# Kernel optimization log

Hardware: AMD Instinct MI355X
Metric: run time of the kernel (lower is better)

The kernel has to match this reference:

```python
import jax, jax.numpy as jnp
import numpy as np

B, S, D, E, H = 8, 1024, 1024, 8, 4096  # batch, seq, n_embd, num_experts, 4*n_embd


def setup_inputs() -> dict:
    key = jax.random.key(0)
    ks = jax.random.split(key, 8)
    sc = 0.02
    return {
        "x": jax.random.normal(ks[0], (B, S, D), jnp.float32),
        "noise": jax.random.normal(ks[1], (B, S, E), jnp.float32),
        "Wg": jax.random.normal(ks[2], (D, E), jnp.float32) * sc,
        "bg": jnp.zeros((E,), jnp.float32),
        "Wn": jax.random.normal(ks[3], (D, E), jnp.float32) * sc,
        "bn": jnp.zeros((E,), jnp.float32),
        "W1": jax.random.normal(ks[4], (E, D, H), jnp.float32) * sc,
        "b1": jnp.zeros((E, H), jnp.float32),
        "W2": jax.random.normal(ks[5], (E, H, D), jnp.float32) * sc,
        "b2": jnp.zeros((E, D), jnp.float32),
        "top_k": 2,
    }


def reference(x, noise, Wg, bg, Wn, bn, W1, b1, W2, b2, top_k):
    # --- NoisyTopkRouter ---
    logits = jnp.einsum("bsd,de->bse", x, Wg) + bg
    noise_logits = jnp.einsum("bsd,de->bse", x, Wn) + bn
    noisy = logits + noise * jax.nn.softplus(noise_logits)  # [B,S,E]
    _, idx = jax.lax.top_k(noisy, top_k)  # [B,S,K]
    in_topk = jax.nn.one_hot(idx, noisy.shape[-1], dtype=noisy.dtype).sum(-2) > 0
    sparse_logits = jnp.where(in_topk, noisy, -jnp.inf)
    gating = jax.nn.softmax(sparse_logits, axis=-1)  # zero outside top-k

    # --- dispatch/combine: gating is exactly zero for non-selected experts,
    # so per-expert masked gather + weighted scatter-add == gated dense sum ---
    g_e = jnp.moveaxis(gating, -1, 0)  # [E,B,S]

    def body(acc, params):
        W1e, b1e, W2e, b2e, ge = params
        h = jax.nn.relu(jnp.einsum("bsd,dh->bsh", x, W1e) + b1e)  # [B,S,H]
        y = (jnp.einsum("bsh,hd->bsd", h, W2e) + b2e) * ge[..., None]
        return acc + y, y

    final_output, expert_outputs = jax.lax.scan(
        body, jnp.zeros_like(x), (W1, b1, W2, b2, g_e)
    )
    # expert_outputs: [E,B,S,D], matching the per-expert weighted outputs list
    return final_output, expert_outputs, gating
```

## Files before the change

### kernel.cpp

```cpp
#include <hip/hip_runtime.h>
#include <hip/hip_bf16.h>
#include <stdint.h>

#define TKN   8192
#define DD    1024
#define EE    8
#define HH    4096
#define TOPK  2
#define NASG  (TKN * TOPK)
#define NSLOT 72

typedef unsigned short u16;
typedef __bf16 bf16x8 __attribute__((ext_vector_type(8)));
typedef float  f32x4  __attribute__((ext_vector_type(4)));

__device__ __forceinline__ u16 f2bf(float f) {
  __hip_bfloat16 h = __float2bfloat16(f);
  return __builtin_bit_cast(u16, h);
}

__device__ __forceinline__ void glds16(const void* g, void* l) {
  __builtin_amdgcn_global_load_lds(
      (__attribute__((address_space(1))) void*)g,
      (__attribute__((address_space(3))) void*)l, 16, 0, 0);
}

#define FENCE() asm volatile("" ::: "memory")
#define BAR()   do { FENCE(); __builtin_amdgcn_s_barrier(); FENCE(); } while (0)
#define VMCNT8() asm volatile("s_waitcnt vmcnt(8)" ::: "memory")
#define VMCNT0() asm volatile("s_waitcnt vmcnt(0)" ::: "memory")

__global__ __launch_bounds__(256) void transpose_cvt_kernel(
    const float* __restrict__ src, u16* __restrict__ dst, int R, int C) {
  __shared__ float tile[32][33];
  int e = blockIdx.z;
  int c0 = blockIdx.x * 32, r0 = blockIdx.y * 32;
  int tx = threadIdx.x, ty = threadIdx.y;
  const float* s = src + (size_t)e * R * C;
  u16* d = dst + (size_t)e * R * C;
#pragma unroll
  for (int j = 0; j < 4; j++)
    tile[ty * 4 + j][tx] = s[(size_t)(r0 + ty * 4 + j) * C + c0 + tx];
  __syncthreads();
#pragma unroll
  for (int j = 0; j < 4; j++)
    d[(size_t)(c0 + ty * 4 + j) * R + r0 + tx] = f2bf(tile[tx][ty * 4 + j]);
}

__global__ __launch_bounds__(256) void router_kernel(
    const float* __restrict__ x, const float* __restrict__ noise,
    const float* __restrict__ Wg, const float* __restrict__ bg,
    const float* __restrict__ Wn, const float* __restrict__ bn,
    float* __restrict__ gating, u16* __restrict__ xb,
    int* __restrict__ sel_e, float* __restrict__ sel_g) {
  int t = blockIdx.x;
  int tid = threadIdx.x;
  float acc[16];
#pragma unroll
  for (int j = 0; j < 16; j++) acc[j] = 0.f;
  for (int i = tid; i < DD; i += 256) {
    float xv = x[(size_t)t * DD + i];
    xb[(size_t)t * DD + i] = f2bf(xv);
    const float4* g4 = (const float4*)(Wg + (size_t)i * EE);
    const float4* n4 = (const float4*)(Wn + (size_t)i * EE);
    float4 ga = g4[0], gb = g4[1];
    float4 na = n4[0], nb = n4[1];
    acc[0] += xv * ga.x;  acc[1] += xv * ga.y;  acc[2] += xv * ga.z;  acc[3] += xv * ga.w;
    acc[4] += xv * gb.x;  acc[5] += xv * gb.y;  acc[6] += xv * gb.z;  acc[7] += xv * gb.w;
    acc[8] += xv * na.x;  acc[9] += xv * na.y;  acc[10] += xv * na.z; acc[11] += xv * na.w;
    acc[12] += xv * nb.x; acc[13] += xv * nb.y; acc[14] += xv * nb.z; acc[15] += xv * nb.w;
  }
  __shared__ float red[4][16];
  int lane = tid & 63, wv = tid >> 6;
#pragma unroll
  for (int j = 0; j < 16; j++) {
    float v = acc[j];
    for (int o = 32; o > 0; o >>= 1) v += __shfl_down(v, o);
    acc[j] = v;
  }
  if (lane == 0) {
#pragma unroll
    for (int j = 0; j < 16; j++) red[wv][j] = acc[j];
  }
  __syncthreads();
  if (tid == 0) {
    float nz[EE];
#pragma unroll
    for (int e = 0; e < EE; e++) {
      float dg = red[0][e] + red[1][e] + red[2][e] + red[3][e] + bg[e];
      float dn = red[0][8 + e] + red[1][8 + e] + red[2][8 + e] + red[3][8 + e] + bn[e];
      float sp = fmaxf(dn, 0.f) + log1pf(expf(-fabsf(dn)));
      nz[e] = dg + noise[(size_t)t * EE + e] * sp;
    }
    int m1 = 0;
    for (int e = 1; e < EE; e++) if (nz[e] > nz[m1]) m1 = e;
    int m2 = (m1 == 0) ? 1 : 0;
    for (int e = 0; e < EE; e++) if (e != m1 && nz[e] > nz[m2]) m2 = e;
    float eb = expf(nz[m2] - nz[m1]);
    float den = 1.f + eb;
    float g1 = 1.f / den, g2 = eb / den;
    gating[(size_t)t * EE + m1] = g1;
    gating[(size_t)t * EE + m2] = g2;
    sel_e[t * 2] = m1; sel_e[t * 2 + 1] = m2;
    sel_g[t * 2] = g1; sel_g[t * 2 + 1] = g2;
  }
}

__global__ __launch_bounds__(256) void hist_scan_kernel(
    const int* __restrict__ sel_e, int* __restrict__ counts,
    int* __restrict__ offsets, int* __restrict__ cursors,
    int* __restrict__ slots) {
  __shared__ int hist[EE];
  int tid = threadIdx.x;
  if (tid < EE) hist[tid] = 0;
  __syncthreads();
  for (int i = tid; i < NASG; i += 256) atomicAdd(&hist[sel_e[i]], 1);
  __syncthreads();
  if (tid == 0) {
    int off = 0, ns = 0;
    for (int e = 0; e < EE; e++) {
      int c = hist[e];
      counts[e] = c; offsets[e] = off; cursors[e] = off; off += c;
      int nrt = (c + 255) >> 8;
      for (int rt = 0; rt < nrt; rt++) slots[ns++] = (e << 16) | rt;
    }
    for (; ns < NSLOT; ns++) slots[ns] = -1;
  }
}

__global__ __launch_bounds__(256) void build_lists_kernel(
    const int* __restrict__ sel_e, const float* __restrict__ sel_g,
    int* __restrict__ cursors, int* __restrict__ tok_list,
    float* __restrict__ gate_list) {
  int t = blockIdx.x * 256 + threadIdx.x;
  int lane = threadIdx.x & 63;
#pragma unroll
  for (int k = 0; k < TOPK; k++) {
    int e = sel_e[t * 2 + k];
    float g = sel_g[t * 2 + k];
    for (int ee = 0; ee < EE; ee++) {
      unsigned long long m = __ballot(e == ee);
      if (m) {
        int leader = __ffsll(m) - 1;
        int base = 0;
        if (lane == leader) base = atomicAdd(&cursors[ee], __popcll(m));
        base = __shfl(base, leader);
        if (e == ee) {
          int slot = base + __popcll(m & ((1ull << lane) - 1ull));
          tok_list[slot] = t;
          gate_list[slot] = g;
        }
      }
    }
  }
}

__global__ __launch_bounds__(256) void zerofill_kernel(
    const float* __restrict__ gating, float* __restrict__ expert_out) {
  int id = blockIdx.x;
  int e = id >> 13, t = id & (TKN - 1);
  if (gating[(size_t)t * EE + e] != 0.f) return;
  float4* p = (float4*)(expert_out + ((size_t)e * TKN + t) * DD);
  p[threadIdx.x] = (float4){0.f, 0.f, 0.f, 0.f};
}

__global__ __launch_bounds__(256) void combine_kernel(
    const float* __restrict__ expert_out, const int* __restrict__ sel_e,
    float* __restrict__ final_out) {
  int t = blockIdx.x;
  int e1 = sel_e[2 * t], e2 = sel_e[2 * t + 1];
  const float4* r1 = (const float4*)(expert_out + ((size_t)e1 * TKN + t) * DD);
  const float4* r2 = (const float4*)(expert_out + ((size_t)e2 * TKN + t) * DD);
  float4* o = (float4*)(final_out + (size_t)t * DD);
  int i = threadIdx.x;
  float4 a = r1[i], b = r2[i];
  o[i] = (float4){a.x + b.x, a.y + b.y, a.z + b.z, a.w + b.w};
}

template<int KLEN, bool GATHER, bool EPI2, int LOGC>
__global__ __launch_bounds__(512, 2) void gemm8_kernel(
    const u16* __restrict__ A, const u16* __restrict__ Bm,
    const float* __restrict__ bias, const int* __restrict__ tok_list,
    const float* __restrict__ gate_list, const int* __restrict__ counts,
    const int* __restrict__ offsets, const int* __restrict__ slots,
    int Ncols, u16* __restrict__ OutBf, float* __restrict__ expert_out) {
  constexpr int NT = KLEN / 64;
  int gid = blockIdx.x;
  int q = gid >> 3;
  int slot = (gid & 7) * 9 + (q >> LOGC);
  int ct = q & ((1 << LOGC) - 1);
  int packed = slots[slot];
  if (packed < 0) return;
  int e = packed >> 16;
  int rt = packed & 0xffff;
  int cnt = counts[e];
  int off = offsets[e];
  int col0 = ct * 256;

  __shared__ __attribute__((aligned(16))) char ldsc[131072];

  int tid = threadIdx.x;
  int w = tid >> 6, l = tid & 63;
  int wm = w >> 2, wn = w & 3;
  int fr = l & 15, hi = l >> 4;
  int kk16 = hi << 4;
  int xr = (fr & 7) << 4;

  int rl0 = w * 8 + (l >> 3);
  int slotE = ((l & 7) ^ ((l >> 3) & 7)) << 3;
  const u16* aptr[4];
  const u16* bptr[4];
#pragma unroll
  for (int i = 0; i < 4; i++) {
    int r = rt * 256 + rl0 + i * 64;
    if (GATHER) {
      int idx = min(off + r, NASG - 1);
      aptr[i] = A + (size_t)tok_list[idx] * KLEN + slotE;
    } else {
      aptr[i] = A + (size_t)(off + r) * KLEN + slotE;
    }
    bptr[i] = Bm + ((size_t)e * Ncols + col0 + rl0 + i * 64) * KLEN + slotE;
  }
  char* ldsA = ldsc;
  char* ldsB = ldsc + 65536;

  auto issueA = [&](int t, int h) {
    char* d = ldsA + (t & 1) * 32768 + h * 16384 + w * 1024;
    glds16(aptr[h * 2 + 0] + t * 64, d);
    glds16(aptr[h * 2 + 1] + t * 64, d + 8192);
  };
  auto issueB = [&](int t, int h) {
    char* d = ldsB + (t & 1) * 32768 + h * 16384 + w * 1024;
    glds16(bptr[h * 2 + 0] + t * 64, d);
    glds16(bptr[h * 2 + 1] + t * 64, d + 8192);
  };

  f32x4 acc[8][4];
#pragma unroll
  for (int m = 0; m < 8; m++)
#pragma unroll
    for (int n = 0; n < 4; n++) acc[m][n] = (f32x4){0.f, 0.f, 0.f, 0.f};
  bf16x8 aF[4][2], bF0[2][2], bF1[2][2];

  issueB(0, 0); issueB(0, 1); issueA(0, 0); issueA(0, 1);
  issueB(1, 0); issueB(1, 1); issueA(1, 0); issueA(1, 1);
  VMCNT8();
  BAR();

  for (int t = 0; t < NT; t++) {
    int abase = (t & 1) * 32768;
    int bbase = 65536 + (t & 1) * 32768;
#pragma unroll
    for (int mm = 0; mm < 4; mm++)
#pragma unroll
      for (int ks = 0; ks < 2; ks++)
        aF[mm][ks] = *(const bf16x8*)(ldsc + abase + (wm * 128 + mm * 16 + fr) * 128 +
                                      ((ks * 64 + kk16) ^ xr));
#pragma unroll
    for (int nn = 0; nn < 2; nn++)
#pragma unroll
      for (int ks = 0; ks < 2; ks++)
        bF0[nn][ks] = *(const bf16x8*)(ldsc + bbase + (wn * 64 + nn * 16 + fr) * 128 +
                                       ((ks * 64 + kk16) ^ xr));
    BAR();
    __builtin_amdgcn_s_setprio(1);
#pragma unroll
    for (int mm = 0; mm < 4; mm++)
#pragma unroll
      for (int nn = 0; nn < 2; nn++)
#pragma unroll
        for (int ks = 0; ks < 2; ks++)
          acc[mm][nn] = __builtin_amdgcn_mfma_f32_16x16x32_bf16(aF[mm][ks], bF0[nn][ks], acc[mm][nn], 0, 0, 0);
    __builtin_amdgcn_s_setprio(0);
    BAR();
#pragma unroll
    for (int nn = 0; nn < 2; nn++)
#pragma unroll
      for (int ks = 0; ks < 2; ks++)
        bF1[nn][ks] = *(const bf16x8*)(ldsc + bbase + (wn * 64 + 32 + nn * 16 + fr) * 128 +
                                       ((ks * 64 + kk16) ^ xr));
    BAR();
    __builtin_amdgcn_s_setprio(1);
#pragma unroll
    for (int mm = 0; mm < 4; mm++)
#pragma unroll
      for (int nn = 0; nn < 2; nn++)
#pragma unroll
        for (int ks = 0; ks < 2; ks++)
          acc[mm][2 + nn] = __builtin_amdgcn_mfma_f32_16x16x32_bf16(aF[mm][ks], bF1[nn][ks], acc[mm][2 + nn], 0, 0, 0);
    __builtin_amdgcn_s_setprio(0);
    BAR();
#pragma unroll
    for (int mm = 0; mm < 4; mm++)
#pragma unroll
      for (int ks = 0; ks < 2; ks++)
        aF[mm][ks] = *(const bf16x8*)(ldsc + abase + (wm * 128 + 64 + mm * 16 + fr) * 128 +
                                      ((ks * 64 + kk16) ^ xr));
    if (t + 2 < NT) { issueB(t + 2, 0); issueB(t + 2, 1); }
    BAR();
    __builtin_amdgcn_s_setprio(1);
#pragma unroll
    for (int mm = 0; mm < 4; mm++)
#pragma unroll
      for (int nn = 0; nn < 2; nn++)
#pragma unroll
        for (int ks = 0; ks < 2; ks++)
          acc[4 + mm][nn] = __builtin_amdgcn_mfma_f32_16x16x32_bf16(aF[mm][ks], bF0[nn][ks], acc[4 + mm][nn], 0, 0, 0);
    __builtin_amdgcn_s_setprio(0);
    BAR();
    if (t + 2 < NT) {
      issueA(t + 2, 0); issueA(t + 2, 1);
      VMCNT8();
    } else {
      VMCNT0();
    }
    BAR();
    __builtin_amdgcn_s_setprio(1);
#pragma unroll
    for (int mm = 0; mm < 4; mm++)
#pragma unroll
      for (int nn = 0; nn < 2; nn++)
#pragma unroll
        for (int ks = 0; ks < 2; ks++)
          acc[4 + mm][2 + nn] = __builtin_amdgcn_mfma_f32_16x16x32_bf16(aF[mm][ks], bF1[nn][ks], acc[4 + mm][2 + nn], 0, 0, 0);
    __builtin_amdgcn_s_setprio(0);
    BAR();
  }

  float biasN[4];
  int cN[4];
#pragma unroll
  for (int n = 0; n < 4; n++) {
    cN[n] = col0 + wn * 64 + (n >> 1) * 32 + (n & 1) * 16 + fr;
    biasN[n] = bias[e * Ncols + cN[n]];
  }
  if constexpr (!EPI2) {
#pragma unroll
    for (int m = 0; m < 8; m++) {
      int rb = rt * 256 + wm * 128 + (m >> 2) * 64 + (m & 3) * 16 + hi * 4;
#pragma unroll
      for (int j = 0; j < 4; j++) {
        int r = rb + j;
        if (r < cnt) {
#pragma unroll
          for (int n = 0; n < 4; n++) {
            float v = acc[m][n][j] + biasN[n];
            OutBf[(size_t)(off + r) * Ncols + cN[n]] = f2bf(fmaxf(v, 0.f));
          }
        }
      }
    }
  } else {
#pragma unroll
    for (int m = 0; m < 8; m++) {
      int rb = rt * 256 + wm * 128 + (m >> 2) * 64 + (m & 3) * 16 + hi * 4;
#pragma unroll
      for (int j = 0; j < 4; j++) {
        int r = rb + j;
        if (r < cnt) {
          int idx = off + r;
          int tok = tok_list[idx];
          float g = gate_list[idx];
          size_t erow = ((size_t)e * TKN + tok) * DD;
#pragma unroll
          for (int n = 0; n < 4; n++)
            expert_out[erow + cN[n]] = (acc[m][n][j] + biasN[n]) * g;
        }
      }
    }
  }
}

extern "C" void kernel_launch(void* const* d_in, const int* in_sizes, int n_in,
                              void* d_out, int out_size, void* d_ws, size_t ws_size,
                              hipStream_t stream) {
  const float* x     = (const float*)d_in[0];
  const float* noise = (const float*)d_in[1];
  const float* Wg    = (const float*)d_in[2];
  const float* bg    = (const float*)d_in[3];
  const float* Wn    = (const float*)d_in[4];
  const float* bn    = (const float*)d_in[5];
  const float* W1    = (const float*)d_in[6];
  const float* b1    = (const float*)d_in[7];
  const float* W2    = (const float*)d_in[8];
  const float* b2    = (const float*)d_in[9];

  float* final_out  = (float*)d_out;
  float* expert_out = final_out + (size_t)TKN * DD;
  float* gating     = expert_out + (size_t)EE * TKN * DD;

  char* ws = (char*)d_ws;
  size_t o = 0;
  auto alloc = [&](size_t bytes) {
    char* p = ws + o;
    o += bytes;
    o = (o + 255) & ~(size_t)255;
    return p;
  };
  u16*   xb        = (u16*)alloc((size_t)TKN * DD * 2);
  u16*   w1t       = (u16*)alloc((size_t)EE * HH * DD * 2);
  u16*   w2t       = (u16*)alloc((size_t)EE * DD * HH * 2);
  u16*   hbuf      = (u16*)alloc(((size_t)NASG + 256) * HH * 2);
  int*   tok_list  = (int*)alloc((size_t)NASG * 4);
  float* gate_list = (float*)alloc((size_t)NASG * 4);
  int*   sel_e     = (int*)alloc((size_t)NASG * 4);
  float* sel_g     = (float*)alloc((size_t)NASG * 4);
  int*   counts    = (int*)alloc(256);
  int*   offsets   = (int*)alloc(256);
  int*   cursors   = (int*)alloc(256);
  int*   slots     = (int*)alloc(NSLOT * 4);

  hipMemsetAsync(gating, 0, (size_t)TKN * EE * sizeof(float), stream);

  router_kernel<<<TKN, 256, 0, stream>>>(x, noise, Wg, bg, Wn, bn, gating, xb, sel_e, sel_g);
  hist_scan_kernel<<<1, 256, 0, stream>>>(sel_e, counts, offsets, cursors, slots);
  build_lists_kernel<<<TKN / 256, 256, 0, stream>>>(sel_e, sel_g, cursors, tok_list, gate_list);
  zerofill_kernel<<<EE * TKN, 256, 0, stream>>>(gating, expert_out);

  transpose_cvt_kernel<<<dim3(HH / 32, DD / 32, EE), dim3(32, 8), 0, stream>>>(W1, w1t, DD, HH);
  transpose_cvt_kernel<<<dim3(DD / 32, HH / 32, EE), dim3(32, 8), 0, stream>>>(W2, w2t, HH, DD);

  gemm8_kernel<DD, true, false, 4><<<8 * 9 * 16, 512, 0, stream>>>(
      xb, w1t, b1, tok_list, nullptr, counts, offsets, slots, HH, hbuf, nullptr);
  gemm8_kernel<HH, false, true, 2><<<8 * 9 * 4, 512, 0, stream>>>(
      hbuf, w2t, b2, tok_list, gate_list, counts, offsets, slots, DD, nullptr, expert_out);

  combine_kernel<<<TKN, 256, 0, stream>>>(expert_out, sel_e, final_out);
}
```

Baseline: 670.5 us.

## Split-K the second expert GEMM and merge partials in a fused combine kernel

The down-projection GEMM is split into four K chunks, which quadruples its block count to fill more CUs. Each chunk writes fp32 partial sums to a workspace buffer. A new merge kernel sums the partials, adds the bias, applies the gate, and writes both the expert outputs and the final combined output. The weight transpose-convert kernel is also widened to 64-row tiles with packed 32-bit bf16 stores. The cost is about 256MB of extra partial-sum traffic, and the old path is kept as a fallback when the workspace is too small.

After: 668.1 us. About the same (-0.3%).

```diff
diff --git a/kernel.cpp b/kernel.cpp
--- a/kernel.cpp
+++ b/kernel.cpp
@@ -32,19 +32,23 @@
 
 __global__ __launch_bounds__(256) void transpose_cvt_kernel(
     const float* __restrict__ src, u16* __restrict__ dst, int R, int C) {
-  __shared__ float tile[32][33];
+  __shared__ float tile[64][33];
   int e = blockIdx.z;
-  int c0 = blockIdx.x * 32, r0 = blockIdx.y * 32;
+  int c0 = blockIdx.x * 32, r0 = blockIdx.y * 64;
   int tx = threadIdx.x, ty = threadIdx.y;
   const float* s = src + (size_t)e * R * C;
-  u16* d = dst + (size_t)e * R * C;
-#pragma unroll
-  for (int j = 0; j < 4; j++)
-    tile[ty * 4 + j][tx] = s[(size_t)(r0 + ty * 4 + j) * C + c0 + tx];
+  uint32_t* d32 = (uint32_t*)(dst + (size_t)e * R * C);
+#pragma unroll
+  for (int j = 0; j < 8; j++)
+    tile[ty * 8 + j][tx] = s[(size_t)(r0 + ty * 8 + j) * C + c0 + tx];
   __syncthreads();
 #pragma unroll
-  for (int j = 0; j < 4; j++)
-    d[(size_t)(c0 + ty * 4 + j) * R + r0 + tx] = f2bf(tile[tx][ty * 4 + j]);
+  for (int jj = 0; jj < 4; jj++) {
+    int c = c0 + ty * 4 + jj;
+    uint32_t lo = f2bf(tile[2 * tx][ty * 4 + jj]);
+    uint32_t hi = f2bf(tile[2 * tx + 1][ty * 4 + jj]);
+    d32[((size_t)c * R + r0) / 2 + tx] = lo | (hi << 16);
+  }
 }
 
 __global__ __launch_bounds__(256) void router_kernel(
@@ -131,7 +135,7 @@
 __global__ __launch_bounds__(256) void build_lists_kernel(
     const int* __restrict__ sel_e, const float* __restrict__ sel_g,
     int* __restrict__ cursors, int* __restrict__ tok_list,
-    float* __restrict__ gate_list) {
+    float* __restrict__ gate_list, int* __restrict__ asg_of) {
   int t = blockIdx.x * 256 + threadIdx.x;
   int lane = threadIdx.x & 63;
 #pragma unroll
@@ -149,6 +153,7 @@
           int slot = base + __popcll(m & ((1ull << lane) - 1ull));
           tok_list[slot] = t;
           gate_list[slot] = g;
+          asg_of[t * 2 + k] = slot;
         }
       }
     }
@@ -177,18 +182,49 @@
   o[i] = (float4){a.x + b.x, a.y + b.y, a.z + b.z, a.w + b.w};
 }
 
-template<int KLEN, bool GATHER, bool EPI2, int LOGC>
+__global__ __launch_bounds__(256) void merge_combine_kernel(
+    const float* __restrict__ part, const int* __restrict__ asg_of,
+    const int* __restrict__ sel_e, const float* __restrict__ sel_g,
+    const float* __restrict__ b2, float* __restrict__ expert_out,
+    float* __restrict__ final_out) {
+  int t = blockIdx.x;
+  int i = threadIdx.x;
+  int i1 = asg_of[2 * t], i2 = asg_of[2 * t + 1];
+  int e1 = sel_e[2 * t], e2 = sel_e[2 * t + 1];
+  float g1 = sel_g[2 * t], g2 = sel_g[2 * t + 1];
+  float4 s1 = {0.f, 0.f, 0.f, 0.f}, s2 = {0.f, 0.f, 0.f, 0.f};
+#pragma unroll
+  for (int kq = 0; kq < 4; kq++) {
+    float4 a = ((const float4*)(part + ((size_t)kq * NASG + i1) * DD))[i];
+    float4 b = ((const float4*)(part + ((size_t)kq * NASG + i2) * DD))[i];
+    s1.x += a.x; s1.y += a.y; s1.z += a.z; s1.w += a.w;
+    s2.x += b.x; s2.y += b.y; s2.z += b.z; s2.w += b.w;
+  }
+  float4 bb1 = ((const float4*)(b2 + (size_t)e1 * DD))[i];
+  float4 bb2 = ((const float4*)(b2 + (size_t)e2 * DD))[i];
+  float4 y1 = {(s1.x + bb1.x) * g1, (s1.y + bb1.y) * g1, (s1.z + bb1.z) * g1, (s1.w + bb1.w) * g1};
+  float4 y2 = {(s2.x + bb2.x) * g2, (s2.y + bb2.y) * g2, (s2.z + bb2.z) * g2, (s2.w + bb2.w) * g2};
+  ((float4*)(expert_out + ((size_t)e1 * TKN + t) * DD))[i] = y1;
+  ((float4*)(expert_out + ((size_t)e2 * TKN + t) * DD))[i] = y2;
+  ((float4*)(final_out + (size_t)t * DD))[i] =
+      (float4){y1.x + y2.x, y1.y + y2.y, y1.z + y2.z, y1.w + y2.w};
+}
+
+template<int KLOOP, int KSTRIDE, bool GATHER, int EPI, int LOGC, int LOGK>
 __global__ __launch_bounds__(512, 2) void gemm8_kernel(
     const u16* __restrict__ A, const u16* __restrict__ Bm,
     const float* __restrict__ bias, const int* __restrict__ tok_list,
     const float* __restrict__ gate_list, const int* __restrict__ counts,
     const int* __restrict__ offsets, const int* __restrict__ slots,
-    int Ncols, u16* __restrict__ OutBf, float* __restrict__ expert_out) {
-  constexpr int NT = KLEN / 64;
+    int Ncols, u16* __restrict__ OutBf, float* __restrict__ outF) {
+  constexpr int NT = KLOOP / 64;
   int gid = blockIdx.x;
   int q = gid >> 3;
-  int slot = (gid & 7) * 9 + (q >> LOGC);
-  int ct = q & ((1 << LOGC) - 1);
+  constexpr int PERX = 9 << LOGC;
+  int kq = q / PERX;
+  int r0q = q - kq * PERX;
+  int slot = (gid & 7) * 9 + (r0q >> LOGC);
+  int ct = r0q & ((1 << LOGC) - 1);
   int packed = slots[slot];
   if (packed < 0) return;
   int e = packed >> 16;
@@ -196,6 +232,7 @@
   int cnt = counts[e];
   int off = offsets[e];
   int col0 = ct * 256;
+  int k0e = kq * KLOOP;
 
   __shared__ __attribute__((aligned(16))) char ldsc[131072];
 
@@ -215,11 +252,11 @@
     int r = rt * 256 + rl0 + i * 64;
     if (GATHER) {
       int idx = min(off + r, NASG - 1);
-      aptr[i] = A + (size_t)tok_list[idx] * KLEN + slotE;
+      aptr[i] = A + (size_t)tok_list[idx] * KSTRIDE + k0e + slotE;
     } else {
-      aptr[i] = A + (size_t)(off + r) * KLEN + slotE;
-    }
-    bptr[i] = Bm + ((size_t)e * Ncols + col0 + rl0 + i * 64) * KLEN + slotE;
+      aptr[i] = A + (size_t)(off + r) * KSTRIDE + k0e + slotE;
+    }
+    bptr[i] = Bm + ((size_t)e * Ncols + col0 + rl0 + i * 64) * KSTRIDE + k0e + slotE;
   }
   char* ldsA = ldsc;
   char* ldsB = ldsc + 65536;
@@ -332,9 +369,9 @@
 #pragma unroll
   for (int n = 0; n < 4; n++) {
     cN[n] = col0 + wn * 64 + (n >> 1) * 32 + (n & 1) * 16 + fr;
-    biasN[n] = bias[e * Ncols + cN[n]];
-  }
-  if constexpr (!EPI2) {
+    biasN[n] = (EPI == 2) ? 0.f : bias[e * Ncols + cN[n]];
+  }
+  if constexpr (EPI == 0) {
 #pragma unroll
     for (int m = 0; m < 8; m++) {
       int rb = rt * 256 + wm * 128 + (m >> 2) * 64 + (m & 3) * 16 + hi * 4;
@@ -350,7 +387,7 @@
         }
       }
     }
-  } else {
+  } else if constexpr (EPI == 1) {
 #pragma unroll
     for (int m = 0; m < 8; m++) {
       int rb = rt * 256 + wm * 128 + (m >> 2) * 64 + (m & 3) * 16 + hi * 4;
@@ -364,7 +401,22 @@
           size_t erow = ((size_t)e * TKN + tok) * DD;
 #pragma unroll
           for (int n = 0; n < 4; n++)
-            expert_out[erow + cN[n]] = (acc[m][n][j] + biasN[n]) * g;
+            outF[erow + cN[n]] = (acc[m][n][j] + biasN[n]) * g;
+        }
+      }
+    }
+  } else {
+#pragma unroll
+    for (int m = 0; m < 8; m++) {
+      int rb = rt * 256 + wm * 128 + (m >> 2) * 64 + (m & 3) * 16 + hi * 4;
+#pragma unroll
+      for (int j = 0; j < 4; j++) {
+        int r = rb + j;
+        if (r < cnt) {
+          size_t prow = ((size_t)kq * NASG + off + r) * DD;
+#pragma unroll
+          for (int n = 0; n < 4; n++)
+            outF[prow + cN[n]] = acc[m][n][j];
         }
       }
     }
@@ -405,25 +457,36 @@
   float* gate_list = (float*)alloc((size_t)NASG * 4);
   int*   sel_e     = (int*)alloc((size_t)NASG * 4);
   float* sel_g     = (float*)alloc((size_t)NASG * 4);
+  int*   asg_of    = (int*)alloc((size_t)NASG * 4);
   int*   counts    = (int*)alloc(256);
   int*   offsets   = (int*)alloc(256);
   int*   cursors   = (int*)alloc(256);
   int*   slots     = (int*)alloc(NSLOT * 4);
+  float* part      = (float*)alloc((size_t)4 * NASG * DD * 4);
+  bool use_split = (o <= ws_size);
 
   hipMemsetAsync(gating, 0, (size_t)TKN * EE * sizeof(float), stream);
 
   router_kernel<<<TKN, 256, 0, stream>>>(x, noise, Wg, bg, Wn, bn, gating, xb, sel_e, sel_g);
   hist_scan_kernel<<<1, 256, 0, stream>>>(sel_e, counts, offsets, cursors, slots);
-  build_lists_kernel<<<TKN / 256, 256, 0, stream>>>(sel_e, sel_g, cursors, tok_list, gate_list);
+  build_lists_kernel<<<TKN / 256, 256, 0, stream>>>(sel_e, sel_g, cursors, tok_list,
+                                                    gate_list, asg_of);
   zerofill_kernel<<<EE * TKN, 256, 0, stream>>>(gating, expert_out);
 
-  transpose_cvt_kernel<<<dim3(HH / 32, DD / 32, EE), dim3(32, 8), 0, stream>>>(W1, w1t, DD, HH);
-  transpose_cvt_kernel<<<dim3(DD / 32, HH / 32, EE), dim3(32, 8), 0, stream>>>(W2, w2t, HH, DD);
-
-  gemm8_kernel<DD, true, false, 4><<<8 * 9 * 16, 512, 0, stream>>>(
+  transpose_cvt_kernel<<<dim3(HH / 32, DD / 64, EE), dim3(32, 8), 0, stream>>>(W1, w1t, DD, HH);
+  transpose_cvt_kernel<<<dim3(DD / 32, HH / 64, EE), dim3(32, 8), 0, stream>>>(W2, w2t, HH, DD);
+
+  gemm8_kernel<DD, DD, true, 0, 4, 0><<<8 * 9 * 16, 512, 0, stream>>>(
       xb, w1t, b1, tok_list, nullptr, counts, offsets, slots, HH, hbuf, nullptr);
-  gemm8_kernel<HH, false, true, 2><<<8 * 9 * 4, 512, 0, stream>>>(
-      hbuf, w2t, b2, tok_list, gate_list, counts, offsets, slots, DD, nullptr, expert_out);
-
-  combine_kernel<<<TKN, 256, 0, stream>>>(expert_out, sel_e, final_out);
-}
+
+  if (use_split) {
+    gemm8_kernel<HH / 4, HH, false, 2, 2, 2><<<8 * 9 * 4 * 4, 512, 0, stream>>>(
+        hbuf, w2t, b2, tok_list, gate_list, counts, offsets, slots, DD, nullptr, part);
+    merge_combine_kernel<<<TKN, 256, 0, stream>>>(part, asg_of, sel_e, sel_g, b2,
+                                                  expert_out, final_out);
+  } else {
+    gemm8_kernel<HH, HH, false, 1, 2, 0><<<8 * 9 * 4, 512, 0, stream>>>(
+        hbuf, w2t, b2, tok_list, gate_list, counts, offsets, slots, DD, nullptr, expert_out);
+    combine_kernel<<<TKN, 256, 0, stream>>>(expert_out, sel_e, final_out);
+  }
+}
```
